# Kernel optimization log

Measured on AMD Instinct MI355X. Metric: run time of the kernel, lower is better.

The kernel has to match this reference:

```python
import jax, jax.numpy as jnp
import numpy as np

H = 100          # LSTM hidden_dim
DATA_DIM = 1500  # max_action_top(100) * max_last_action(15)
OUT = 130
B = 32           # len_batch
S = 32           # slice_index (uniform segment length)
N = 2 * B * S
RIN = 1024 + 512  # n_flatten + 512


def setup_inputs() -> dict:
    key = jax.random.key(0)
    ks = iter(jax.random.split(key, 48))
    def p(shape, s=0.05):
        return jax.random.normal(next(ks), shape, dtype=jnp.float32) * s
    inp = {
        'observations': p((N, 3, 64, 64), 1.0),
        'data': p((N, DATA_DIM), 1.0),
        'conv1_w': p((32, 3, 8, 8)), 'conv1_b': p((32,)),
        'conv2_w': p((64, 32, 4, 4)), 'conv2_b': p((64,)),
        'conv3_w': p((64, 64, 3, 3)), 'conv3_b': p((64,)),
        'lin1_w': p((1024, DATA_DIM)), 'lin1_b': p((1024,)),
        'lin2_w': p((512, 1024)), 'lin2_b': p((512,)),
        'rnns_wih0': p((4 * H, RIN)), 'rnns_whh0': p((4 * H, H)), 'rnns_bih0': p((4 * H,)), 'rnns_bhh0': p((4 * H,)),
        'rnns_wih1': p((4 * H, H)), 'rnns_whh1': p((4 * H, H)), 'rnns_bih1': p((4 * H,)), 'rnns_bhh1': p((4 * H,)),
        'rnn_wih0': p((4 * H, RIN)), 'rnn_whh0': p((4 * H, H)), 'rnn_bih0': p((4 * H,)), 'rnn_bhh0': p((4 * H,)),
        'rnn_wih1': p((4 * H, H)), 'rnn_whh1': p((4 * H, H)), 'rnn_bih1': p((4 * H,)), 'rnn_bhh1': p((4 * H,)),
        'fc1_w': p((512, 2 * H)), 'fc1_b': p((512,)),
        'fc2_w': p((OUT, 512)), 'fc2_b': p((OUT,)),
        'slice_index': S,
        'len_batch': B,
    }
    return inp


def _conv(x, w, b, stride):
    # NCHW / OIHW, VALID padding (padding=0 in torch)
    y = jax.lax.conv_general_dilated(x, w, (stride, stride), 'VALID')
    return y + b[None, :, None, None]


def _lstm_layer(x, w_ih, w_hh, b_ih, b_hh, h0, c0):
    # x: [B, S, in]; torch gate order: i, f, g, o
    bias = b_ih + b_hh
    def step(carry, x_t):
        h, c = carry
        g = x_t @ w_ih.T + h @ w_hh.T + bias
        i, f, gg, o = jnp.split(g, 4, axis=-1)
        c = jax.nn.sigmoid(f) * c + jax.nn.sigmoid(i) * jnp.tanh(gg)
        h = jax.nn.sigmoid(o) * jnp.tanh(c)
        return (h, c), h
    (hT, cT), hs = jax.lax.scan(step, (h0, c0), jnp.swapaxes(x, 0, 1))
    return jnp.swapaxes(hs, 0, 1), hT, cT


def _lstm2(x, prm, h0, c0):
    # prm: (wih0, whh0, bih0, bhh0, wih1, whh1, bih1, bhh1); h0, c0: [2, B, H]
    y0, h0f, c0f = _lstm_layer(x, prm[0], prm[1], prm[2], prm[3], h0[0], c0[0])
    y1, h1f, c1f = _lstm_layer(y0, prm[4], prm[5], prm[6], prm[7], h0[1], c0[1])
    return y1, jnp.stack([h0f, h1f]), jnp.stack([c0f, c1f])


def reference(observations, data,
              conv1_w, conv1_b, conv2_w, conv2_b, conv3_w, conv3_b,
              lin1_w, lin1_b, lin2_w, lin2_b,
              rnns_wih0, rnns_whh0, rnns_bih0, rnns_bhh0,
              rnns_wih1, rnns_whh1, rnns_bih1, rnns_bhh1,
              rnn_wih0, rnn_whh0, rnn_bih0, rnn_bhh0,
              rnn_wih1, rnn_whh1, rnn_bih1, rnn_bhh1,
              fc1_w, fc1_b, fc2_w, fc2_b,
              slice_index, len_batch):
    x = jax.nn.relu(_conv(observations, conv1_w, conv1_b, 4))
    x = jax.nn.relu(_conv(x, conv2_w, conv2_b, 2))
    x = jax.nn.relu(_conv(x, conv3_w, conv3_b, 1))
    c_out = x.reshape(x.shape[0], -1)  # [N, 1024]
    d_out = jax.nn.relu(data @ lin1_w.T + lin1_b) @ lin2_w.T + lin2_b  # [N, 512]
    feat = jnp.concatenate([c_out, d_out], axis=-1)  # [N, 1536]
    segs = feat.reshape(2 * len_batch, slice_index, feat.shape[-1])  # [2B, S, 1536]
    prm_s = (rnns_wih0, rnns_whh0, rnns_bih0, rnns_bhh0, rnns_wih1, rnns_whh1, rnns_bih1, rnns_bhh1)
    prm = (rnn_wih0, rnn_whh0, rnn_bih0, rnn_bhh0, rnn_wih1, rnn_whh1, rnn_bih1, rnn_bhh1)
    z = jnp.zeros((2, len_batch, H), dtype=feat.dtype)
    out_s, hn, cn = _lstm2(segs[:len_batch], prm_s, z, z)      # zero init, as in loop
    out, _, _ = _lstm2(segs[len_batch:], prm, hn, cn)          # carries (hn, cn) from rnn_s
    out_in = jnp.concatenate([out[:, -1, :], out_s[:, -1, :]], axis=-1)  # [B, 200]
    return jax.nn.relu(out_in @ fc1_w.T + fc1_b) @ fc2_w.T + fc2_b       # [B, OUT]
```

## Files before the change

kernel.cpp:

```cpp
#include <hip/hip_runtime.h>
#include <hip/hip_fp16.h>
#include <math.h>


typedef __attribute__((ext_vector_type(4))) float f32x4;
typedef __attribute__((ext_vector_type(8))) short s16x8;
typedef __attribute__((ext_vector_type(8))) unsigned short u16x8;
typedef __attribute__((ext_vector_type(4))) unsigned int u32x4;

__device__ __forceinline__ unsigned short f2bf(float f){
  union { float f; unsigned int u; } v; v.f = f;
  unsigned int r = (v.u + 0x7fffu + ((v.u >> 16) & 1u)) >> 16;
  return (unsigned short)r;
}
__device__ __forceinline__ unsigned short f2h(float f){
  return __half_as_ushort(__float2half(f));
}
__device__ __forceinline__ float sigmoidf_(float x){ return 1.0f/(1.0f+__expf(-x)); }
__device__ __forceinline__ float tanhf_(float x){
  float e = __expf(-2.0f*fabsf(x));
  float t = (1.0f - e)/(1.0f + e);
  return copysignf(t, x);
}

#if __has_builtin(__builtin_amdgcn_fdot2)
typedef _Float16 f16x2 __attribute__((ext_vector_type(2)));
__device__ __forceinline__ float dot2h(unsigned int a, unsigned int b, float c){
  union { unsigned int u; f16x2 h; } ua, ub;
  ua.u = a; ub.u = b;
  return __builtin_amdgcn_fdot2(ua.h, ub.h, c, false);
}
#else
__device__ __forceinline__ float dot2h(unsigned int a, unsigned int b, float c){
  __half2 ha = *(__half2*)&a, hb = *(__half2*)&b;
  float2 fa = __half22float2(ha), fb = __half22float2(hb);
  return c + fa.x*fb.x + fa.y*fb.y;
}
#endif

__global__ void prep_k(
    const float* __restrict__ data, unsigned short* __restrict__ data_bf,
    const float* __restrict__ l1w,  unsigned short* __restrict__ l1w_bf,
    const float* __restrict__ l2w,  unsigned short* __restrict__ l2w_bf,
    const float* __restrict__ c1w,  unsigned short* __restrict__ c1w_bf,
    const float* __restrict__ c2w,  unsigned short* __restrict__ c2w_bf,
    const float* __restrict__ c3w,  unsigned short* __restrict__ c3w_bf,
    const float* __restrict__ wihS, unsigned short* __restrict__ wihS_bf,
    const float* __restrict__ wihR, unsigned short* __restrict__ wihR_bf,
    const float* __restrict__ m0, const float* __restrict__ m1,
    const float* __restrict__ m2, const float* __restrict__ m3,
    const float* __restrict__ m4, const float* __restrict__ m5,
    unsigned int* __restrict__ wpk)
{
  const int job = blockIdx.y;
  const int stride = gridDim.x * blockDim.x;
  int e0 = blockIdx.x * blockDim.x + threadIdx.x;
  if (job == 0){
    for (int e = e0; e < 2048*1536; e += stride){
      int r = e / 1536, k = e - r*1536;
      data_bf[e] = (k < 1500) ? f2bf(data[(size_t)r*1500 + k]) : (unsigned short)0;
    }
  } else if (job == 1){
    for (int e = e0; e < 1024*1536; e += stride){
      int r = e / 1536, k = e - r*1536;
      l1w_bf[e] = (k < 1500) ? f2bf(l1w[(size_t)r*1500 + k]) : (unsigned short)0;
    }
  } else if (job == 2){
    for (int e = e0; e < 512*1024; e += stride) l2w_bf[e] = f2bf(l2w[e]);
  } else if (job == 3){
    for (int e = e0; e < 32*192; e += stride) c1w_bf[e] = f2bf(c1w[e]);
  } else if (job == 4){
    for (int e = e0; e < 64*512; e += stride){
      int oc = e >> 9, r = e & 511;
      int tap = r >> 5, ic = r & 31;
      c2w_bf[e] = f2bf(c2w[(size_t)oc*512 + ic*16 + tap]);
    }
  } else if (job == 5){
    for (int e = e0; e < 64*576; e += stride){
      int oc = e / 576, r = e - oc*576;
      int tap = r >> 6, ic = r & 63;
      c3w_bf[e] = f2bf(c3w[(size_t)oc*576 + ic*9 + tap]);
    }
  } else if (job == 6 || job == 7){
    const float* src = (job == 6) ? wihS : wihR;
    unsigned short* dst = (job == 6) ? wihS_bf : wihR_bf;
    for (int e = e0; e < 400*1536; e += stride){
      int g = e / 1536, k = e - g*1536;
      int ksrc = (k < 1024) ? ((k & 63)*16 + (k >> 6)) : k;
      dst[e] = f2bf(src[(size_t)g*1536 + ksrc]);
    }
  } else {
    const float* srcs[6] = {m0,m1,m2,m3,m4,m5};
    for (int e = e0; e < 6*20000; e += stride){
      int mat = e / 20000, r = e - mat*20000;
      int kk = r / 400, g = r - kk*400;
      const float* src = srcs[mat];
      unsigned int lo = f2h(src[g*100 + 2*kk]);
      unsigned int hi = f2h(src[g*100 + 2*kk + 1]);
      wpk[e] = lo | (hi << 16);
    }
  }
}

template<int BM,int BN,int WAVES_M,int WAVES_N,int AMODE,int CMODE,int RELU,int NGUARD,
         int CIN,int HI,int WI,int KH,int KW,int ST,int HO,int WO>
__global__ __launch_bounds__(256) void mgemm(
    const void* __restrict__ Av, const unsigned short* __restrict__ B,
    void* __restrict__ Cv, const float* __restrict__ bias,
    int M, int N, int K, int lda, int ldc, int cstride)
{
  constexpr int BK = 64;
  constexpr int WROWS = BM / WAVES_M;
  constexpr int WCOLS = BN / WAVES_N;
  constexpr int MF = WROWS / 16;
  constexpr int NF = WCOLS / 16;
  constexpr int HOWO = HO*WO;
  __shared__ unsigned short As[BM*BK];
  __shared__ unsigned short Bs[BN*BK];
  const int tid = threadIdx.x;
  const int bm = blockIdx.x * BM;
  const int bn = blockIdx.y * BN;
  const int lane = tid & 63, w = tid >> 6;
  const int wm = w / WAVES_N, wn = w % WAVES_N;
  const int m0 = wm * WROWS, n0 = wn * WCOLS;

  f32x4 acc[MF][NF] = {};

  const int ar = tid >> 1;
  const int as0 = 4 * (tid & 1);
  const int row_g = bm + ar;
  int a_n = 0, a_oy = 0, a_ox = 0;
  if (AMODE != 0){ a_n = row_g / HOWO; int p = row_g - a_n*HOWO; a_oy = p / WO; a_ox = p - a_oy*WO; }
// ... 87 lines not shown
  } else {
    unsigned short* tile = As;
    #pragma unroll
    for (int i = 0; i < MF; ++i)
      #pragma unroll
      for (int j = 0; j < NF; ++j){
        int col = n0 + j*16 + (lane & 15);
        float bv = bias ? bias[bn + col] : 0.f;
        #pragma unroll
        for (int q = 0; q < 4; ++q){
          int row = m0 + i*16 + (lane >> 4)*4 + q;
          float v = acc[i][j][q] + bv;
          if (RELU) v = fmaxf(v, 0.f);
          tile[row*BN + col] = f2bf(v);
        }
      }
    __syncthreads();
    unsigned short* Cu = (unsigned short*)Cv;
    constexpr int CHUNKS = (BM*BN)/(256*8);
    #pragma unroll
    for (int c = 0; c < CHUNKS; ++c){
      int flat = tid*8 + c*2048;
      int row = flat / BN, col = flat - (flat/BN)*BN;
      u16x8 v = *(const u16x8*)&tile[flat];
      int rg = bm + row;
      size_t addr;
      if constexpr (CMODE == 0) addr = (size_t)rg*ldc + bn + col;
      else { int n = rg >> 4, p = rg & 15; addr = (size_t)n*cstride + p*64 + col; }
      *(u16x8*)&Cu[addr] = v;
    }
  }
}

__global__ __launch_bounds__(256,1) void lstm_k(
    const float* __restrict__ X0s, const float* __restrict__ X0r,
    const unsigned int* __restrict__ wpk,
    const float* __restrict__ s_bih0, const float* __restrict__ s_bhh0,
    const float* __restrict__ s_bih1, const float* __restrict__ s_bhh1,
    const float* __restrict__ r_bih0, const float* __restrict__ r_bhh0,
    const float* __restrict__ r_bih1, const float* __restrict__ r_bhh1,
    const float* __restrict__ f1w, const float* __restrict__ f1b,
    const float* __restrict__ f2w, const float* __restrict__ f2b,
    float* __restrict__ out)
{
  __shared__ alignas(16) unsigned int h0p[2][56];
  __shared__ alignas(16) unsigned int h1p[2][56];
  __shared__ alignas(16) unsigned int hbufp[1792];
  __shared__ alignas(16) float Xl1[12800];
  __shared__ float xin[200];
  __shared__ float mid[512];

  const int b = blockIdx.x, tid = threadIdx.x;
  const int e = tid >> 1, sub = tid & 1;
  const bool act = (e < 100);
  const int eS = act ? e : 0;
  const int gA = sub*100 + eS;
  const int gB = gA + 200;

  if (tid < 56){ h0p[0][tid]=0u; h0p[1][tid]=0u; h1p[0][tid]=0u; h1p[1][tid]=0u; }
  for (int q = tid; q < 1792; q += 256) hbufp[q] = 0u;
  float c0r = 0.f, c1r = 0.f;
  __syncthreads();

  #pragma unroll 1
  for (int s = 0; s < 2; ++s){
    const float* Xp = (s ? X0r : X0s) + (size_t)b*32*400;
    const unsigned int* w0P  = wpk + (size_t)(s ? 3 : 0)*20000;
    const unsigned int* w1xP = wpk + (size_t)(s ? 4 : 1)*20000;
    const unsigned int* w1hP = wpk + (size_t)(s ? 5 : 2)*20000;
    const float* bi0 = s ? r_bih0 : s_bih0;
    const float* bh0 = s ? r_bhh0 : s_bhh0;
    const float* bi1 = s ? r_bih1 : s_bih1;
    const float* bh1 = s ? r_bhh1 : s_bhh1;

    {
      unsigned int wA[50], wB[50];
      #pragma unroll
      for (int p = 0; p < 50; ++p){
        wA[p] = w0P[p*400 + gA];
        wB[p] = w0P[p*400 + gB];
      }
      float bsA = bi0[gA] + bh0[gA];
      float bsB = bi0[gB] + bh0[gB];
      float xcA = Xp[gA], xcB = Xp[gB], xnA, xnB;
      #pragma unroll 1
      for (int t = 0; t < 32; ++t){
        if (t < 31){ xnA = Xp[(t+1)*400 + gA]; xnB = Xp[(t+1)*400 + gB]; }
        const u32x4* h4 = (const u32x4*)h0p[t & 1];
        float a0=0.f, a1=0.f, b0=0.f, b1=0.f;
        #pragma unroll
        for (int i = 0; i < 12; ++i){
          u32x4 hv = h4[i];
          a0 = dot2h(wA[4*i+0], hv[0], a0);
          a1 = dot2h(wA[4*i+1], hv[1], a1);
          a0 = dot2h(wA[4*i+2], hv[2], a0);
          a1 = dot2h(wA[4*i+3], hv[3], a1);
          b0 = dot2h(wB[4*i+0], hv[0], b0);
          b1 = dot2h(wB[4*i+1], hv[1], b1);
          b0 = dot2h(wB[4*i+2], hv[2], b0);
          b1 = dot2h(wB[4*i+3], hv[3], b1);
        }
        { u32x4 hv = h4[12];
          a0 = dot2h(wA[48], hv[0], a0);
          a1 = dot2h(wA[49], hv[1], a1);
          b0 = dot2h(wB[48], hv[0], b0);
          b1 = dot2h(wB[49], hv[1], b1);
        }
        float preA = (a0 + a1) + xcA + bsA;
        float preB = (b0 + b1) + xcB + bsB;
        float vA = sigmoidf_(preA);
        float vB = sub ? sigmoidf_(preB) : tanhf_(preB);
        float send = vA * vB;
        float recv = __shfl_xor(send, 1);
        if (act && sub){
          c0r = vA*c0r + recv;
          float hn = vB * tanhf_(c0r);
          unsigned short hv16 = f2h(hn);
          ((unsigned short*)h0p[(t+1) & 1])[e] = hv16;
          ((unsigned short*)hbufp)[t*112 + e] = hv16;
        }
        xcA = xnA; xcB = xnB;
        __syncthreads();
      }
    }
    {
      unsigned int wA[50], wB[50];
      #pragma unroll
      for (int p = 0; p < 50; ++p){
        wA[p] = w1xP[p*400 + gA];
        wB[p] = w1xP[p*400 + gB];
      }
      float bsA = bi1[gA] + bh1[gA];
      float bsB = bi1[gB] + bh1[gB];
      #pragma unroll 1
      for (int t = 0; t < 32; ++t){
        const u32x4* x4 = (const u32x4*)&hbufp[t*56];
        float a0=0.f, a1=0.f, b0=0.f, b1=0.f;
        #pragma unroll
        for (int i = 0; i < 12; ++i){
          u32x4 hv = x4[i];
          a0 = dot2h(wA[4*i+0], hv[0], a0);
          a1 = dot2h(wA[4*i+1], hv[1], a1);
          a0 = dot2h(wA[4*i+2], hv[2], a0);
          a1 = dot2h(wA[4*i+3], hv[3], a1);
          b0 = dot2h(wB[4*i+0], hv[0], b0);
          b1 = dot2h(wB[4*i+1], hv[1], b1);
          b0 = dot2h(wB[4*i+2], hv[2], b0);
          b1 = dot2h(wB[4*i+3], hv[3], b1);
        }
        { u32x4 hv = x4[12];
          a0 = dot2h(wA[48], hv[0], a0);
          a1 = dot2h(wA[49], hv[1], a1);
          b0 = dot2h(wB[48], hv[0], b0);
          b1 = dot2h(wB[49], hv[1], b1);
        }
        if (act){
          Xl1[t*400 + gA] = (a0 + a1) + bsA;
          Xl1[t*400 + gB] = (b0 + b1) + bsB;
        }
      }
    }
    {
      unsigned int wA[50], wB[50];
      #pragma unroll
      for (int p = 0; p < 50; ++p){
        wA[p] = w1hP[p*400 + gA];
        wB[p] = w1hP[p*400 + gB];
      }
      #pragma unroll 1
      for (int t = 0; t < 32; ++t){
        const u32x4* h4 = (const u32x4*)h1p[t & 1];
        float a0=0.f, a1=0.f, b0=0.f, b1=0.f;
        #pragma unroll
        for (int i = 0; i < 12; ++i){
          u32x4 hv = h4[i];
          a0 = dot2h(wA[4*i+0], hv[0], a0);
          a1 = dot2h(wA[4*i+1], hv[1], a1);
          a0 = dot2h(wA[4*i+2], hv[2], a0);
          a1 = dot2h(wA[4*i+3], hv[3], a1);
          b0 = dot2h(wB[4*i+0], hv[0], b0);
          b1 = dot2h(wB[4*i+1], hv[1], b1);
          b0 = dot2h(wB[4*i+2], hv[2], b0);
          b1 = dot2h(wB[4*i+3], hv[3], b1);
        }
        { u32x4 hv = h4[12];
          a0 = dot2h(wA[48], hv[0], a0);
          a1 = dot2h(wA[49], hv[1], a1);
          b0 = dot2h(wB[48], hv[0], b0);
          b1 = dot2h(wB[49], hv[1], b1);
        }
        float preA = (a0 + a1) + Xl1[t*400 + gA];
        float preB = (b0 + b1) + Xl1[t*400 + gB];
        float vA = sigmoidf_(preA);
        float vB = sub ? sigmoidf_(preB) : tanhf_(preB);
        float send = vA * vB;
        float recv = __shfl_xor(send, 1);
        if (act && sub){
          c1r = vA*c1r + recv;
          float hn = vB * tanhf_(c1r);
          ((unsigned short*)h1p[(t+1) & 1])[e] = f2h(hn);
          if (t == 31){
            if (s) xin[e] = hn;
            else   xin[100 + e] = hn;
          }
        }
        __syncthreads();
      }
    }
  }

  for (int r = tid; r < 512; r += 256){
    float acc = f1b[r];
    const float* wrow = f1w + (size_t)r*200;
    #pragma unroll 4
    for (int k = 0; k < 200; ++k) acc += xin[k]*wrow[k];
    mid[r] = fmaxf(acc, 0.f);
  }
  __syncthreads();
  if (tid < 130){
    float acc = f2b[tid];
    const float* wrow = f2w + (size_t)tid*512;
    #pragma unroll 4
    for (int k = 0; k < 512; ++k) acc += mid[k]*wrow[k];
    out[b*130 + tid] = acc;
  }
}

extern "C" void kernel_launch(void* const* d_in, const int* in_sizes, int n_in,
                              void* d_out, int out_size, void* d_ws, size_t ws_size,
                              hipStream_t stream)
{
  const float* obs  = (const float*)d_in[0];
  const float* data = (const float*)d_in[1];
  const float* c1w = (const float*)d_in[2];  const float* c1b = (const float*)d_in[3];
  const float* c2w = (const float*)d_in[4];  const float* c2b = (const float*)d_in[5];
  const float* c3w = (const float*)d_in[6];  const float* c3b = (const float*)d_in[7];
  const float* l1w = (const float*)d_in[8];  const float* l1b = (const float*)d_in[9];
  const float* l2w = (const float*)d_in[10]; const float* l2b = (const float*)d_in[11];
  const float* s_wih0=(const float*)d_in[12]; const float* s_whh0=(const float*)d_in[13];
  const float* s_bih0=(const float*)d_in[14]; const float* s_bhh0=(const float*)d_in[15];
  const float* s_wih1=(const float*)d_in[16]; const float* s_whh1=(const float*)d_in[17];
  const float* s_bih1=(const float*)d_in[18]; const float* s_bhh1=(const float*)d_in[19];
  const float* r_wih0=(const float*)d_in[20]; const float* r_whh0=(const float*)d_in[21];
  const float* r_bih0=(const float*)d_in[22]; const float* r_bhh0=(const float*)d_in[23];
  const float* r_wih1=(const float*)d_in[24]; const float* r_whh1=(const float*)d_in[25];
  const float* r_bih1=(const float*)d_in[26]; const float* r_bhh1=(const float*)d_in[27];
  const float* f1w=(const float*)d_in[28]; const float* f1b=(const float*)d_in[29];
  const float* f2w=(const float*)d_in[30]; const float* f2b=(const float*)d_in[31];
  float* out = (float*)d_out;
  (void)in_sizes; (void)n_in; (void)out_size;

  char* p = (char*)d_ws;
  auto alloc = [&](size_t bytes){ void* r = (void*)p; p += (bytes + 255) & ~(size_t)255; return r; };
  unsigned short* data_bf = (unsigned short*)alloc((size_t)2048*1536*2);
  unsigned short* c1w_bf  = (unsigned short*)alloc((size_t)32*192*2);
  unsigned short* c2w_bf  = (unsigned short*)alloc((size_t)64*512*2);
  unsigned short* c3w_bf  = (unsigned short*)alloc((size_t)64*576*2);
  unsigned short* l1w_bf  = (unsigned short*)alloc((size_t)1024*1536*2);
  unsigned short* l2w_bf  = (unsigned short*)alloc((size_t)512*1024*2);
  unsigned short* wihS_bf = (unsigned short*)alloc((size_t)400*1536*2);
  unsigned short* wihR_bf = (unsigned short*)alloc((size_t)400*1536*2);
  unsigned short* conv1o  = (unsigned short*)alloc((size_t)2048*225*32*2);
  unsigned short* conv2o  = (unsigned short*)alloc((size_t)2048*36*64*2);
  unsigned short* feat    = (unsigned short*)alloc((size_t)2048*1536*2);
  unsigned short* lin1o   = (unsigned short*)alloc((size_t)2048*1024*2);
  float* X0s  = (float*)alloc((size_t)1024*400*4);
  float* X0r  = (float*)alloc((size_t)1024*400*4);
  unsigned int* wpk = (unsigned int*)alloc((size_t)6*20000*4);
  (void)ws_size;

  prep_k<<<dim3(512,9),256,0,stream>>>(
      data, data_bf, l1w, l1w_bf, l2w, l2w_bf, c1w, c1w_bf,
      c2w, c2w_bf, c3w, c3w_bf, s_wih0, wihS_bf, r_wih0, wihR_bf,
      s_whh0, s_wih1, s_whh1, r_whh0, r_wih1, r_whh1, wpk);

  mgemm<128,32,4,1, 1,0,1,0, 3,64,64,8,8,4,15,15><<<dim3(3600,1),256,0,stream>>>(
      obs, c1w_bf, conv1o, c1b, 460800, 32, 192, 0, 32, 0);
  mgemm<128,64,2,2, 2,0,1,0, 32,15,15,4,4,2,6,6><<<dim3(576,1),256,0,stream>>>(
      conv1o, c2w_bf, conv2o, c2b, 73728, 64, 512, 0, 64, 0);
  mgemm<128,64,2,2, 0,0,1,0, 1,1,1,1,1,1,1,1><<<dim3(16,16),256,0,stream>>>(
      data_bf, l1w_bf, lin1o, l1b, 2048, 1024, 1536, 1536, 1024, 0);
  mgemm<128,64,2,2, 2,2,1,0, 64,6,6,3,3,1,4,4><<<dim3(256,1),256,0,stream>>>(
      conv2o, c3w_bf, feat, c3b, 32768, 64, 576, 0, 0, 1536);
  mgemm<128,64,2,2, 0,0,0,0, 1,1,1,1,1,1,1,1><<<dim3(16,8),256,0,stream>>>(
      lin1o, l2w_bf, feat + 1024, l2b, 2048, 512, 1024, 1024, 1536, 0);
  mgemm<128,64,2,2, 0,3,0,1, 1,1,1,1,1,1,1,1><<<dim3(8,7),256,0,stream>>>(
      feat, wihS_bf, X0s, (const float*)nullptr, 1024, 400, 1536, 1536, 400, 0);
  mgemm<128,64,2,2, 0,3,0,1, 1,1,1,1,1,1,1,1><<<dim3(8,7),256,0,stream>>>(
      feat + (size_t)1024*1536, wihR_bf, X0r, (const float*)nullptr, 1024, 400, 1536, 1536, 400, 0);

  lstm_k<<<32,256,0,stream>>>(X0s, X0r, wpk,
                              s_bih0,s_bhh0,s_bih1,s_bhh1,
                              r_bih0,r_bhh0,r_bih1,r_bhh1,
                              f1w, f1b, f2w, f2b, out);
}
```

Before: 331.5 us.

## Pipeline LSTM layers 0 and 1 across two thread groups in one block

The LSTM kernel now runs 512 threads: the first 256 compute layer 0 and the second 256 compute layer 1 one timestep behind, in a wavefront schedule. The three sequential passes (layer 0 recurrence, layer 1 input projection buffered in shared memory, layer 1 recurrence) become one loop of 33 steps. This removes the hbufp and Xl1 shared buffers and roughly halves the serial step count. In exchange, layer-1 threads hold 200 packed weight registers each, which risks spills under launch bounds of 512 threads, and layer 1 does twice the dot products per step.

```diff
diff --git a/kernel.cpp b/kernel.cpp
--- a/kernel.cpp
+++ b/kernel.cpp
@@ -251,7 +251,7 @@
   }
 }
 
-__global__ __launch_bounds__(256,1) void lstm_k(
+__global__ __launch_bounds__(512,2) void lstm_k(
     const float* __restrict__ X0s, const float* __restrict__ X0r,
     const unsigned int* __restrict__ wpk,
     const float* __restrict__ s_bih0, const float* __restrict__ s_bhh0,
@@ -264,20 +264,19 @@
 {
   __shared__ alignas(16) unsigned int h0p[2][56];
   __shared__ alignas(16) unsigned int h1p[2][56];
-  __shared__ alignas(16) unsigned int hbufp[1792];
-  __shared__ alignas(16) float Xl1[12800];
   __shared__ float xin[200];
   __shared__ float mid[512];
 
   const int b = blockIdx.x, tid = threadIdx.x;
-  const int e = tid >> 1, sub = tid & 1;
+  const bool isL0 = (tid < 256);
+  const int tl = isL0 ? tid : (tid - 256);
+  const int e = tl >> 1, sub = tl & 1;
   const bool act = (e < 100);
   const int eS = act ? e : 0;
   const int gA = sub*100 + eS;
   const int gB = gA + 200;
 
   if (tid < 56){ h0p[0][tid]=0u; h0p[1][tid]=0u; h1p[0][tid]=0u; h1p[1][tid]=0u; }
-  for (int q = tid; q < 1792; q += 256) hbufp[q] = 0u;
   float c0r = 0.f, c1r = 0.f;
   __syncthreads();
 
@@ -292,148 +291,134 @@
     const float* bi1 = s ? r_bih1 : s_bih1;
     const float* bh1 = s ? r_bhh1 : s_bhh1;
 
-    {
-      unsigned int wA[50], wB[50];
+    unsigned int wreg[200];
+    float bsA, bsB, xcA = 0.f, xcB = 0.f;
+    if (isL0){
       #pragma unroll
       for (int p = 0; p < 50; ++p){
-        wA[p] = w0P[p*400 + gA];
-        wB[p] = w0P[p*400 + gB];
-      }
-      float bsA = bi0[gA] + bh0[gA];
-      float bsB = bi0[gB] + bh0[gB];
-      float xcA = Xp[gA], xcB = Xp[gB], xnA, xnB;
-      #pragma unroll 1
-      for (int t = 0; t < 32; ++t){
-        if (t < 31){ xnA = Xp[(t+1)*400 + gA]; xnB = Xp[(t+1)*400 + gB]; }
-        const u32x4* h4 = (const u32x4*)h0p[t & 1];
-        float a0=0.f, a1=0.f, b0=0.f, b1=0.f;
-        #pragma unroll
-        for (int i = 0; i < 12; ++i){
-          u32x4 hv = h4[i];
-          a0 = dot2h(wA[4*i+0], hv[0], a0);
-          a1 = dot2h(wA[4*i+1], hv[1], a1);
-          a0 = dot2h(wA[4*i+2], hv[2], a0);
-          a1 = dot2h(wA[4*i+3], hv[3], a1);
-          b0 = dot2h(wB[4*i+0], hv[0], b0);
-          b1 = dot2h(wB[4*i+1], hv[1], b1);
-          b0 = dot2h(wB[4*i+2], hv[2], b0);
-          b1 = dot2h(wB[4*i+3], hv[3], b1);
+        wreg[p]      = w0P[p*400 + gA];
+        wreg[50+p]   = w0P[p*400 + gB];
+      }
+      bsA = bi0[gA] + bh0[gA];
+      bsB = bi0[gB] + bh0[gB];
+      xcA = Xp[gA]; xcB = Xp[gB];
+    } else {
+      #pragma unroll
+      for (int p = 0; p < 50; ++p){
+        wreg[p]      = w1hP[p*400 + gA];
+        wreg[50+p]   = w1hP[p*400 + gB];
+        wreg[100+p]  = w1xP[p*400 + gA];
+        wreg[150+p]  = w1xP[p*400 + gB];
+      }
+      bsA = bi1[gA] + bh1[gA];
+      bsB = bi1[gB] + bh1[gB];
+    }
+    __syncthreads();
+
+    #pragma unroll 1
+    for (int t = 0; t < 33; ++t){
+      if (isL0){
+        if (t < 32){
+          float xnA = 0.f, xnB = 0.f;
+          if (t < 31){ xnA = Xp[(t+1)*400 + gA]; xnB = Xp[(t+1)*400 + gB]; }
+          const u32x4* h4 = (const u32x4*)h0p[t & 1];
+          float a0=0.f, a1=0.f, b0=0.f, b1=0.f;
+          #pragma unroll
+          for (int i = 0; i < 12; ++i){
+            u32x4 hv = h4[i];
+            a0 = dot2h(wreg[4*i+0], hv[0], a0);
+            a1 = dot2h(wreg[4*i+1], hv[1], a1);
+            a0 = dot2h(wreg[4*i+2], hv[2], a0);
+            a1 = dot2h(wreg[4*i+3], hv[3], a1);
+            b0 = dot2h(wreg[50+4*i+0], hv[0], b0);
+            b1 = dot2h(wreg[50+4*i+1], hv[1], b1);
+            b0 = dot2h(wreg[50+4*i+2], hv[2], b0);
+            b1 = dot2h(wreg[50+4*i+3], hv[3], b1);
+          }
+          { u32x4 hv = h4[12];
+            a0 = dot2h(wreg[48], hv[0], a0);
+            a1 = dot2h(wreg[49], hv[1], a1);
+            b0 = dot2h(wreg[98], hv[0], b0);
+            b1 = dot2h(wreg[99], hv[1], b1);
+          }
+          float preA = (a0 + a1) + xcA + bsA;
+          float preB = (b0 + b1) + xcB + bsB;
+          float vA = sigmoidf_(preA);
+          float vB = sub ? sigmoidf_(preB) : tanhf_(preB);
+          float send = vA * vB;
+          float recv = __shfl_xor(send, 1);
+          if (act && sub){
+            c0r = vA*c0r + recv;
+            float hn = vB * tanhf_(c0r);
+            ((unsigned short*)h0p[(t+1) & 1])[e] = f2h(hn);
+          }
+          xcA = xnA; xcB = xnB;
         }
-        { u32x4 hv = h4[12];
-          a0 = dot2h(wA[48], hv[0], a0);
-          a1 = dot2h(wA[49], hv[1], a1);
-          b0 = dot2h(wB[48], hv[0], b0);
-          b1 = dot2h(wB[49], hv[1], b1);
-        }
-        float preA = (a0 + a1) + xcA + bsA;
-        float preB = (b0 + b1) + xcB + bsB;
-        float vA = sigmoidf_(preA);
-        float vB = sub ? sigmoidf_(preB) : tanhf_(preB);
-        float send = vA * vB;
-        float recv = __shfl_xor(send, 1);
-        if (act && sub){
-          c0r = vA*c0r + recv;
-          float hn = vB * tanhf_(c0r);
-          unsigned short hv16 = f2h(hn);
-          ((unsigned short*)h0p[(t+1) & 1])[e] = hv16;
-          ((unsigned short*)hbufp)[t*112 + e] = hv16;
-        }
-        xcA = xnA; xcB = xnB;
-        __syncthreads();
-      }
-    }
-    {
-      unsigned int wA[50], wB[50];
-      #pragma unroll
-      for (int p = 0; p < 50; ++p){
-        wA[p] = w1xP[p*400 + gA];
-        wB[p] = w1xP[p*400 + gB];
-      }
-      float bsA = bi1[gA] + bh1[gA];
-      float bsB = bi1[gB] + bh1[gB];
-      #pragma unroll 1
-      for (int t = 0; t < 32; ++t){
-        const u32x4* x4 = (const u32x4*)&hbufp[t*56];
-        float a0=0.f, a1=0.f, b0=0.f, b1=0.f;
-        #pragma unroll
-        for (int i = 0; i < 12; ++i){
-          u32x4 hv = x4[i];
-          a0 = dot2h(wA[4*i+0], hv[0], a0);
-          a1 = dot2h(wA[4*i+1], hv[1], a1);
-          a0 = dot2h(wA[4*i+2], hv[2], a0);
-          a1 = dot2h(wA[4*i+3], hv[3], a1);
-          b0 = dot2h(wB[4*i+0], hv[0], b0);
-          b1 = dot2h(wB[4*i+1], hv[1], b1);
-          b0 = dot2h(wB[4*i+2], hv[2], b0);
-          b1 = dot2h(wB[4*i+3], hv[3], b1);
-        }
-        { u32x4 hv = x4[12];
-          a0 = dot2h(wA[48], hv[0], a0);
-          a1 = dot2h(wA[49], hv[1], a1);
-          b0 = dot2h(wB[48], hv[0], b0);
-          b1 = dot2h(wB[49], hv[1], b1);
-        }
-        if (act){
-          Xl1[t*400 + gA] = (a0 + a1) + bsA;
-          Xl1[t*400 + gB] = (b0 + b1) + bsB;
-        }
-      }
-    }
-    {
-      unsigned int wA[50], wB[50];
-      #pragma unroll
-      for (int p = 0; p < 50; ++p){
-        wA[p] = w1hP[p*400 + gA];
-        wB[p] = w1hP[p*400 + gB];
-      }
-      #pragma unroll 1
-      for (int t = 0; t < 32; ++t){
-        const u32x4* h4 = (const u32x4*)h1p[t & 1];
-        float a0=0.f, a1=0.f, b0=0.f, b1=0.f;
-        #pragma unroll
-        for (int i = 0; i < 12; ++i){
-          u32x4 hv = h4[i];
-          a0 = dot2h(wA[4*i+0], hv[0], a0);
-          a1 = dot2h(wA[4*i+1], hv[1], a1);
-          a0 = dot2h(wA[4*i+2], hv[2], a0);
-          a1 = dot2h(wA[4*i+3], hv[3], a1);
-          b0 = dot2h(wB[4*i+0], hv[0], b0);
-          b1 = dot2h(wB[4*i+1], hv[1], b1);
-          b0 = dot2h(wB[4*i+2], hv[2], b0);
-          b1 = dot2h(wB[4*i+3], hv[3], b1);
-        }
-        { u32x4 hv = h4[12];
-          a0 = dot2h(wA[48], hv[0], a0);
-          a1 = dot2h(wA[49], hv[1], a1);
-          b0 = dot2h(wB[48], hv[0], b0);
-          b1 = dot2h(wB[49], hv[1], b1);
-        }
-        float preA = (a0 + a1) + Xl1[t*400 + gA];
-        float preB = (b0 + b1) + Xl1[t*400 + gB];
-        float vA = sigmoidf_(preA);
-        float vB = sub ? sigmoidf_(preB) : tanhf_(preB);
-        float send = vA * vB;
-        float recv = __shfl_xor(send, 1);
-        if (act && sub){
-          c1r = vA*c1r + recv;
-          float hn = vB * tanhf_(c1r);
-          ((unsigned short*)h1p[(t+1) & 1])[e] = f2h(hn);
-          if (t == 31){
-            if (s) xin[e] = hn;
-            else   xin[100 + e] = hn;
+      } else {
+        if (t >= 1){
+          const int u = t - 1;
+          const u32x4* h4 = (const u32x4*)h1p[u & 1];
+          const u32x4* x4 = (const u32x4*)h0p[t & 1];
+          float a0=0.f, a1=0.f, b0=0.f, b1=0.f;
+          #pragma unroll
+          for (int i = 0; i < 12; ++i){
+            u32x4 hv = h4[i];
+            a0 = dot2h(wreg[4*i+0], hv[0], a0);
+            a1 = dot2h(wreg[4*i+1], hv[1], a1);
+            a0 = dot2h(wreg[4*i+2], hv[2], a0);
+            a1 = dot2h(wreg[4*i+3], hv[3], a1);
+            b0 = dot2h(wreg[50+4*i+0], hv[0], b0);
+            b1 = dot2h(wreg[50+4*i+1], hv[1], b1);
+            b0 = dot2h(wreg[50+4*i+2], hv[2], b0);
+            b1 = dot2h(wreg[50+4*i+3], hv[3], b1);
+            u32x4 xv = x4[i];
+            a0 = dot2h(wreg[100+4*i+0], xv[0], a0);
+            a1 = dot2h(wreg[100+4*i+1], xv[1], a1);
+            a0 = dot2h(wreg[100+4*i+2], xv[2], a0);
+            a1 = dot2h(wreg[100+4*i+3], xv[3], a1);
+            b0 = dot2h(wreg[150+4*i+0], xv[0], b0);
+            b1 = dot2h(wreg[150+4*i+1], xv[1], b1);
+            b0 = dot2h(wreg[150+4*i+2], xv[2], b0);
+            b1 = dot2h(wreg[150+4*i+3], xv[3], b1);
+          }
+          { u32x4 hv = h4[12];
+            a0 = dot2h(wreg[48], hv[0], a0);
+            a1 = dot2h(wreg[49], hv[1], a1);
+            b0 = dot2h(wreg[98], hv[0], b0);
+            b1 = dot2h(wreg[99], hv[1], b1);
+            u32x4 xv = x4[12];
+            a0 = dot2h(wreg[148], xv[0], a0);
+            a1 = dot2h(wreg[149], xv[1], a1);
+            b0 = dot2h(wreg[198], xv[0], b0);
+            b1 = dot2h(wreg[199], xv[1], b1);
+          }
+          float preA = (a0 + a1) + bsA;
+          float preB = (b0 + b1) + bsB;
+          float vA = sigmoidf_(preA);
+          float vB = sub ? sigmoidf_(preB) : tanhf_(preB);
+          float send = vA * vB;
+          float recv = __shfl_xor(send, 1);
+          if (act && sub){
+            c1r = vA*c1r + recv;
+            float hn = vB * tanhf_(c1r);
+            ((unsigned short*)h1p[t & 1])[e] = f2h(hn);
+            if (u == 31){
+              if (s) xin[e] = hn;
+              else   xin[100 + e] = hn;
+            }
           }
         }
-        __syncthreads();
-      }
+      }
+      __syncthreads();
     }
   }
 
-  for (int r = tid; r < 512; r += 256){
-    float acc = f1b[r];
-    const float* wrow = f1w + (size_t)r*200;
+  {
+    float acc = f1b[tid];
+    const float* wrow = f1w + (size_t)tid*200;
     #pragma unroll 4
     for (int k = 0; k < 200; ++k) acc += xin[k]*wrow[k];
-    mid[r] = fmaxf(acc, 0.f);
+    mid[tid] = fmaxf(acc, 0.f);
   }
   __syncthreads();
   if (tid < 130){
@@ -508,7 +493,7 @@
   mgemm<128,64,2,2, 0,3,0,1, 1,1,1,1,1,1,1,1><<<dim3(8,7),256,0,stream>>>(
       feat + (size_t)1024*1536, wihR_bf, X0r, (const float*)nullptr, 1024, 400, 1536, 1536, 400, 0);
 
-  lstm_k<<<32,256,0,stream>>>(X0s, X0r, wpk,
+  lstm_k<<<32,512,0,stream>>>(X0s, X0r, wpk,
                               s_bih0,s_bhh0,s_bih1,s_bhh1,
                               r_bih0,r_bhh0,r_bih1,r_bhh1,
                               f1w, f1b, f2w, f2b, out);
```

After: 697.3 us. 110% more time.

## Pack four LSTM sequences per 1024-thread block and store layer-1 inputs as fp16

Applied to the files above, without the earlier changes.

The LSTM kernel now runs four batch sequences in one 1024-thread block (8 blocks instead of 32). Each 256-thread slice keeps its own shared-memory hidden-state buffers. The precomputed layer-1 input projections are stored as fp16 instead of fp32 so that four slices fit in LDS. The intent appears to be fewer blocks that share weight fetches through cache. The costs are block-wide barriers across 1024 threads, a 128-VGPR limit per thread that may spill the 100 register-resident weights, and lower precision for the layer-1 inputs.

```diff
diff --git a/kernel.cpp b/kernel.cpp
--- a/kernel.cpp
+++ b/kernel.cpp
@@ -15,6 +15,9 @@
 }
 __device__ __forceinline__ unsigned short f2h(float f){
   return __half_as_ushort(__float2half(f));
+}
+__device__ __forceinline__ float h2f(unsigned short u){
+  return __half2float(__ushort_as_half(u));
 }
 __device__ __forceinline__ float sigmoidf_(float x){ return 1.0f/(1.0f+__expf(-x)); }
 __device__ __forceinline__ float tanhf_(float x){
@@ -251,7 +254,8 @@
   }
 }
 
-__global__ __launch_bounds__(256,1) void lstm_k(
+#define NSEG 4
+__global__ __launch_bounds__(1024,1) void lstm_k(
     const float* __restrict__ X0s, const float* __restrict__ X0r,
     const unsigned int* __restrict__ wpk,
     const float* __restrict__ s_bih0, const float* __restrict__ s_bhh0,
@@ -262,22 +266,25 @@
     const float* __restrict__ f2w, const float* __restrict__ f2b,
     float* __restrict__ out)
 {
-  __shared__ alignas(16) unsigned int h0p[2][56];
-  __shared__ alignas(16) unsigned int h1p[2][56];
-  __shared__ alignas(16) unsigned int hbufp[1792];
-  __shared__ alignas(16) float Xl1[12800];
-  __shared__ float xin[200];
-  __shared__ float mid[512];
-
-  const int b = blockIdx.x, tid = threadIdx.x;
-  const int e = tid >> 1, sub = tid & 1;
+  __shared__ alignas(16) unsigned int h0p[NSEG][2][56];
+  __shared__ alignas(16) unsigned int h1p[NSEG][2][56];
+  __shared__ alignas(16) unsigned int hbufp[NSEG][1792];
+  __shared__ alignas(16) unsigned short Xl1h[NSEG][12800];
+  __shared__ float xin[NSEG][200];
+  __shared__ float mid[NSEG][512];
+
+  const int tid = threadIdx.x;
+  const int sl = tid >> 8;
+  const int tl = tid & 255;
+  const int b = blockIdx.x*NSEG + sl;
+  const int e = tl >> 1, sub = tl & 1;
   const bool act = (e < 100);
   const int eS = act ? e : 0;
   const int gA = sub*100 + eS;
   const int gB = gA + 200;
 
-  if (tid < 56){ h0p[0][tid]=0u; h0p[1][tid]=0u; h1p[0][tid]=0u; h1p[1][tid]=0u; }
-  for (int q = tid; q < 1792; q += 256) hbufp[q] = 0u;
+  if (tl < 56){ h0p[sl][0][tl]=0u; h0p[sl][1][tl]=0u; h1p[sl][0][tl]=0u; h1p[sl][1][tl]=0u; }
+  for (int q = tl; q < 1792; q += 256) hbufp[sl][q] = 0u;
   float c0r = 0.f, c1r = 0.f;
   __syncthreads();
 
@@ -305,7 +312,7 @@
       #pragma unroll 1
       for (int t = 0; t < 32; ++t){
         if (t < 31){ xnA = Xp[(t+1)*400 + gA]; xnB = Xp[(t+1)*400 + gB]; }
-        const u32x4* h4 = (const u32x4*)h0p[t & 1];
+        const u32x4* h4 = (const u32x4*)h0p[sl][t & 1];
         float a0=0.f, a1=0.f, b0=0.f, b1=0.f;
         #pragma unroll
         for (int i = 0; i < 12; ++i){
@@ -335,8 +342,8 @@
           c0r = vA*c0r + recv;
           float hn = vB * tanhf_(c0r);
           unsigned short hv16 = f2h(hn);
-          ((unsigned short*)h0p[(t+1) & 1])[e] = hv16;
-          ((unsigned short*)hbufp)[t*112 + e] = hv16;
+          ((unsigned short*)h0p[sl][(t+1) & 1])[e] = hv16;
+          ((unsigned short*)hbufp[sl])[t*112 + e] = hv16;
         }
         xcA = xnA; xcB = xnB;
         __syncthreads();
@@ -353,7 +360,7 @@
       float bsB = bi1[gB] + bh1[gB];
       #pragma unroll 1
       for (int t = 0; t < 32; ++t){
-        const u32x4* x4 = (const u32x4*)&hbufp[t*56];
+        const u32x4* x4 = (const u32x4*)&hbufp[sl][t*56];
         float a0=0.f, a1=0.f, b0=0.f, b1=0.f;
         #pragma unroll
         for (int i = 0; i < 12; ++i){
@@ -374,8 +381,8 @@
           b1 = dot2h(wB[49], hv[1], b1);
         }
         if (act){
-          Xl1[t*400 + gA] = (a0 + a1) + bsA;
-          Xl1[t*400 + gB] = (b0 + b1) + bsB;
+          Xl1h[sl][t*400 + gA] = f2h((a0 + a1) + bsA);
+          Xl1h[sl][t*400 + gB] = f2h((b0 + b1) + bsB);
         }
       }
     }
@@ -388,7 +395,7 @@
       }
       #pragma unroll 1
       for (int t = 0; t < 32; ++t){
-        const u32x4* h4 = (const u32x4*)h1p[t & 1];
+        const u32x4* h4 = (const u32x4*)h1p[sl][t & 1];
         float a0=0.f, a1=0.f, b0=0.f, b1=0.f;
         #pragma unroll
         for (int i = 0; i < 12; ++i){
@@ -408,8 +415,8 @@
           b0 = dot2h(wB[48], hv[0], b0);
           b1 = dot2h(wB[49], hv[1], b1);
         }
-        float preA = (a0 + a1) + Xl1[t*400 + gA];
-        float preB = (b0 + b1) + Xl1[t*400 + gB];
+        float preA = (a0 + a1) + h2f(Xl1h[sl][t*400 + gA]);
+        float preB = (b0 + b1) + h2f(Xl1h[sl][t*400 + gB]);
         float vA = sigmoidf_(preA);
         float vB = sub ? sigmoidf_(preB) : tanhf_(preB);
         float send = vA * vB;
@@ -417,10 +424,10 @@
         if (act && sub){
           c1r = vA*c1r + recv;
           float hn = vB * tanhf_(c1r);
-          ((unsigned short*)h1p[(t+1) & 1])[e] = f2h(hn);
+          ((unsigned short*)h1p[sl][(t+1) & 1])[e] = f2h(hn);
           if (t == 31){
-            if (s) xin[e] = hn;
-            else   xin[100 + e] = hn;
+            if (s) xin[sl][e] = hn;
+            else   xin[sl][100 + e] = hn;
           }
         }
         __syncthreads();
@@ -428,20 +435,20 @@
     }
   }
 
-  for (int r = tid; r < 512; r += 256){
+  for (int r = tl; r < 512; r += 256){
     float acc = f1b[r];
     const float* wrow = f1w + (size_t)r*200;
     #pragma unroll 4
-    for (int k = 0; k < 200; ++k) acc += xin[k]*wrow[k];
-    mid[r] = fmaxf(acc, 0.f);
+    for (int k = 0; k < 200; ++k) acc += xin[sl][k]*wrow[k];
+    mid[sl][r] = fmaxf(acc, 0.f);
   }
   __syncthreads();
-  if (tid < 130){
-    float acc = f2b[tid];
-    const float* wrow = f2w + (size_t)tid*512;
+  if (tl < 130){
+    float acc = f2b[tl];
+    const float* wrow = f2w + (size_t)tl*512;
     #pragma unroll 4
-    for (int k = 0; k < 512; ++k) acc += mid[k]*wrow[k];
-    out[b*130 + tid] = acc;
+    for (int k = 0; k < 512; ++k) acc += mid[sl][k]*wrow[k];
+    out[b*130 + tl] = acc;
   }
 }
 
@@ -508,7 +515,7 @@
   mgemm<128,64,2,2, 0,3,0,1, 1,1,1,1,1,1,1,1><<<dim3(8,7),256,0,stream>>>(
       feat + (size_t)1024*1536, wihR_bf, X0r, (const float*)nullptr, 1024, 400, 1536, 1536, 400, 0);
 
-  lstm_k<<<32,256,0,stream>>>(X0s, X0r, wpk,
+  lstm_k<<<8,1024,0,stream>>>(X0s, X0r, wpk,
                               s_bih0,s_bhh0,s_bih1,s_bhh1,
                               r_bih0,r_bhh0,r_bih1,r_bhh1,
                               f1w, f1b, f2w, f2b, out);
```

New measurement: 1.087 ms. +227.9%, slower.

## Split LSTM into wavefront kernels and move layer-1 input projection to GEMM

Applied to the files above, without the earlier changes.

The single LSTM kernel used to run four recurrences back to back: both layers of rnn_s, then both layers of rnn. It is now split into three recurrence kernels with GEMM launches between them. The layer-1 input projections become bf16 matrix-core GEMMs over the stored layer-0 hidden states, and layer-1 of rnn_s runs in the same launch as layer-0 of rnn. This cuts the serial chain from four 32-step recurrences to three and takes the scalar input projection off the critical path. In exchange it adds more kernel launches, extra global round trips for hidden states, carried state and projections, and bf16 rounding of layer-0 outputs.

```diff
diff --git a/kernel.cpp b/kernel.cpp
--- a/kernel.cpp
+++ b/kernel.cpp
@@ -49,8 +49,16 @@
     const float* __restrict__ wihR, unsigned short* __restrict__ wihR_bf,
     const float* __restrict__ m0, const float* __restrict__ m1,
     const float* __restrict__ m2, const float* __restrict__ m3,
-    const float* __restrict__ m4, const float* __restrict__ m5,
-    unsigned int* __restrict__ wpk)
+    unsigned int* __restrict__ wpk,
+    const float* __restrict__ wih1S, const float* __restrict__ wih1R,
+    unsigned short* __restrict__ w1xS_bf, unsigned short* __restrict__ w1xR_bf,
+    const float* __restrict__ s_bih0, const float* __restrict__ s_bhh0,
+    const float* __restrict__ s_bih1, const float* __restrict__ s_bhh1,
+    const float* __restrict__ r_bih0, const float* __restrict__ r_bhh0,
+    const float* __restrict__ r_bih1, const float* __restrict__ r_bhh1,
+    float* __restrict__ bias0S, float* __restrict__ bias0R,
+    float* __restrict__ bias1S, float* __restrict__ bias1R,
+    unsigned short* __restrict__ h0outS, unsigned short* __restrict__ h0outR)
 {
   const int job = blockIdx.y;
   const int stride = gridDim.x * blockDim.x;
@@ -89,15 +97,35 @@
       int ksrc = (k < 1024) ? ((k & 63)*16 + (k >> 6)) : k;
       dst[e] = f2bf(src[(size_t)g*1536 + ksrc]);
     }
-  } else {
-    const float* srcs[6] = {m0,m1,m2,m3,m4,m5};
-    for (int e = e0; e < 6*20000; e += stride){
+  } else if (job == 8){
+    const float* srcs[4] = {m0,m1,m2,m3};
+    for (int e = e0; e < 4*20000; e += stride){
       int mat = e / 20000, r = e - mat*20000;
       int kk = r / 400, g = r - kk*400;
       const float* src = srcs[mat];
       unsigned int lo = f2h(src[g*100 + 2*kk]);
       unsigned int hi = f2h(src[g*100 + 2*kk + 1]);
       wpk[e] = lo | (hi << 16);
+    }
+  } else if (job == 9){
+    for (int e = e0; e < 2*400*128; e += stride){
+      int half = e / 51200, r = e - half*51200;
+      int g = r >> 7, k = r & 127;
+      const float* src = half ? wih1R : wih1S;
+      unsigned short* dst = half ? w1xR_bf : w1xS_bf;
+      dst[r] = (k < 100) ? f2bf(src[g*100 + k]) : (unsigned short)0;
+    }
+  } else {
+    for (int e = e0; e < 1600 + 131072; e += stride){
+      if (e < 400)        bias0S[e]       = s_bih0[e]       + s_bhh0[e];
+      else if (e < 800)   bias0R[e-400]   = r_bih0[e-400]   + r_bhh0[e-400];
+      else if (e < 1200)  bias1S[e-800]   = s_bih1[e-800]   + s_bhh1[e-800];
+      else if (e < 1600)  bias1R[e-1200]  = r_bih1[e-1200]  + r_bhh1[e-1200];
+      else {
+        int idx = e - 1600;
+        if (idx < 65536) ((unsigned int*)h0outS)[idx] = 0u;
+        else             ((unsigned int*)h0outR)[idx - 65536] = 0u;
+      }
     }
   }
 }
@@ -251,183 +279,142 @@
   }
 }
 
-__global__ __launch_bounds__(256,1) void lstm_k(
-    const float* __restrict__ X0s, const float* __restrict__ X0r,
-    const unsigned int* __restrict__ wpk,
-    const float* __restrict__ s_bih0, const float* __restrict__ s_bhh0,
-    const float* __restrict__ s_bih1, const float* __restrict__ s_bhh1,
-    const float* __restrict__ r_bih0, const float* __restrict__ r_bhh0,
-    const float* __restrict__ r_bih1, const float* __restrict__ r_bhh1,
-    const float* __restrict__ f1w, const float* __restrict__ f1b,
-    const float* __restrict__ f2w, const float* __restrict__ f2b,
-    float* __restrict__ out)
-{
-  __shared__ alignas(16) unsigned int h0p[2][56];
-  __shared__ alignas(16) unsigned int h1p[2][56];
-  __shared__ alignas(16) unsigned int hbufp[1792];
-  __shared__ alignas(16) float Xl1[12800];
-  __shared__ float xin[200];
-  __shared__ float mid[512];
-
-  const int b = blockIdx.x, tid = threadIdx.x;
+__device__ __forceinline__ void rec_body(
+    int seg, int tid,
+    const float* __restrict__ X,
+    const unsigned int* __restrict__ wP,
+    const float* __restrict__ bsum,
+    const float* __restrict__ hinit,
+    const float* __restrict__ cinit,
+    unsigned short* __restrict__ houtm,
+    float* __restrict__ hfin,
+    float* __restrict__ cfin,
+    unsigned int (*hp)[56],
+    float* __restrict__ xout)
+{
   const int e = tid >> 1, sub = tid & 1;
   const bool act = (e < 100);
   const int eS = act ? e : 0;
   const int gA = sub*100 + eS;
   const int gB = gA + 200;
 
-  if (tid < 56){ h0p[0][tid]=0u; h0p[1][tid]=0u; h1p[0][tid]=0u; h1p[1][tid]=0u; }
-  for (int q = tid; q < 1792; q += 256) hbufp[q] = 0u;
-  float c0r = 0.f, c1r = 0.f;
+  if (tid < 56){
+    unsigned int v = 0u;
+    if (hinit && tid < 50){
+      unsigned int lo = f2h(hinit[seg*100 + 2*tid]);
+      unsigned int hi = f2h(hinit[seg*100 + 2*tid + 1]);
+      v = lo | (hi << 16);
+    }
+    hp[0][tid] = v;
+    hp[1][tid] = 0u;
+  }
+  float cr = 0.f;
+  if (cinit && act && sub) cr = cinit[seg*100 + e];
   __syncthreads();
 
+  unsigned int wA[50], wB[50];
+  #pragma unroll
+  for (int p = 0; p < 50; ++p){
+    wA[p] = wP[p*400 + gA];
+    wB[p] = wP[p*400 + gB];
+  }
+  float bsA = bsum ? bsum[gA] : 0.f;
+  float bsB = bsum ? bsum[gB] : 0.f;
+  const float* Xs = X + (size_t)seg*32*400;
+  float xcA = Xs[gA], xcB = Xs[gB], xnA = 0.f, xnB = 0.f;
+  float hnK = 0.f;
+
   #pragma unroll 1
-  for (int s = 0; s < 2; ++s){
-    const float* Xp = (s ? X0r : X0s) + (size_t)b*32*400;
-    const unsigned int* w0P  = wpk + (size_t)(s ? 3 : 0)*20000;
-    const unsigned int* w1xP = wpk + (size_t)(s ? 4 : 1)*20000;
-    const unsigned int* w1hP = wpk + (size_t)(s ? 5 : 2)*20000;
-    const float* bi0 = s ? r_bih0 : s_bih0;
-    const float* bh0 = s ? r_bhh0 : s_bhh0;
-    const float* bi1 = s ? r_bih1 : s_bih1;
-    const float* bh1 = s ? r_bhh1 : s_bhh1;
-
-    {
-      unsigned int wA[50], wB[50];
-      #pragma unroll
-      for (int p = 0; p < 50; ++p){
-        wA[p] = w0P[p*400 + gA];
-        wB[p] = w0P[p*400 + gB];
-      }
-      float bsA = bi0[gA] + bh0[gA];
-      float bsB = bi0[gB] + bh0[gB];
-      float xcA = Xp[gA], xcB = Xp[gB], xnA, xnB;
-      #pragma unroll 1
-      for (int t = 0; t < 32; ++t){
-        if (t < 31){ xnA = Xp[(t+1)*400 + gA]; xnB = Xp[(t+1)*400 + gB]; }
-        const u32x4* h4 = (const u32x4*)h0p[t & 1];
-        float a0=0.f, a1=0.f, b0=0.f, b1=0.f;
-        #pragma unroll
-        for (int i = 0; i < 12; ++i){
-          u32x4 hv = h4[i];
-          a0 = dot2h(wA[4*i+0], hv[0], a0);
-          a1 = dot2h(wA[4*i+1], hv[1], a1);
-          a0 = dot2h(wA[4*i+2], hv[2], a0);
-          a1 = dot2h(wA[4*i+3], hv[3], a1);
-          b0 = dot2h(wB[4*i+0], hv[0], b0);
-          b1 = dot2h(wB[4*i+1], hv[1], b1);
-          b0 = dot2h(wB[4*i+2], hv[2], b0);
-          b1 = dot2h(wB[4*i+3], hv[3], b1);
-        }
-        { u32x4 hv = h4[12];
-          a0 = dot2h(wA[48], hv[0], a0);
-          a1 = dot2h(wA[49], hv[1], a1);
-          b0 = dot2h(wB[48], hv[0], b0);
-          b1 = dot2h(wB[49], hv[1], b1);
-        }
-        float preA = (a0 + a1) + xcA + bsA;
-        float preB = (b0 + b1) + xcB + bsB;
-        float vA = sigmoidf_(preA);
-        float vB = sub ? sigmoidf_(preB) : tanhf_(preB);
-        float send = vA * vB;
-        float recv = __shfl_xor(send, 1);
-        if (act && sub){
-          c0r = vA*c0r + recv;
-          float hn = vB * tanhf_(c0r);
-          unsigned short hv16 = f2h(hn);
-          ((unsigned short*)h0p[(t+1) & 1])[e] = hv16;
-          ((unsigned short*)hbufp)[t*112 + e] = hv16;
-        }
-        xcA = xnA; xcB = xnB;
-        __syncthreads();
-      }
-    }
-    {
-      unsigned int wA[50], wB[50];
-      #pragma unroll
-      for (int p = 0; p < 50; ++p){
-        wA[p] = w1xP[p*400 + gA];
-        wB[p] = w1xP[p*400 + gB];
-      }
-      float bsA = bi1[gA] + bh1[gA];
-      float bsB = bi1[gB] + bh1[gB];
-      #pragma unroll 1
-      for (int t = 0; t < 32; ++t){
-        const u32x4* x4 = (const u32x4*)&hbufp[t*56];
-        float a0=0.f, a1=0.f, b0=0.f, b1=0.f;
-        #pragma unroll
-        for (int i = 0; i < 12; ++i){
-          u32x4 hv = x4[i];
-          a0 = dot2h(wA[4*i+0], hv[0], a0);
-          a1 = dot2h(wA[4*i+1], hv[1], a1);
-          a0 = dot2h(wA[4*i+2], hv[2], a0);
-          a1 = dot2h(wA[4*i+3], hv[3], a1);
-          b0 = dot2h(wB[4*i+0], hv[0], b0);
-          b1 = dot2h(wB[4*i+1], hv[1], b1);
-          b0 = dot2h(wB[4*i+2], hv[2], b0);
-          b1 = dot2h(wB[4*i+3], hv[3], b1);
-        }
-        { u32x4 hv = x4[12];
-          a0 = dot2h(wA[48], hv[0], a0);
-          a1 = dot2h(wA[49], hv[1], a1);
-          b0 = dot2h(wB[48], hv[0], b0);
-          b1 = dot2h(wB[49], hv[1], b1);
-        }
-        if (act){
-          Xl1[t*400 + gA] = (a0 + a1) + bsA;
-          Xl1[t*400 + gB] = (b0 + b1) + bsB;
-        }
-      }
-    }
-    {
-      unsigned int wA[50], wB[50];
-      #pragma unroll
-      for (int p = 0; p < 50; ++p){
-        wA[p] = w1hP[p*400 + gA];
-        wB[p] = w1hP[p*400 + gB];
-      }
-      #pragma unroll 1
-      for (int t = 0; t < 32; ++t){
-        const u32x4* h4 = (const u32x4*)h1p[t & 1];
-        float a0=0.f, a1=0.f, b0=0.f, b1=0.f;
-        #pragma unroll
-        for (int i = 0; i < 12; ++i){
-          u32x4 hv = h4[i];
-          a0 = dot2h(wA[4*i+0], hv[0], a0);
-          a1 = dot2h(wA[4*i+1], hv[1], a1);
-          a0 = dot2h(wA[4*i+2], hv[2], a0);
-          a1 = dot2h(wA[4*i+3], hv[3], a1);
-          b0 = dot2h(wB[4*i+0], hv[0], b0);
-          b1 = dot2h(wB[4*i+1], hv[1], b1);
-          b0 = dot2h(wB[4*i+2], hv[2], b0);
-          b1 = dot2h(wB[4*i+3], hv[3], b1);
-        }
-        { u32x4 hv = h4[12];
-          a0 = dot2h(wA[48], hv[0], a0);
-          a1 = dot2h(wA[49], hv[1], a1);
-          b0 = dot2h(wB[48], hv[0], b0);
-          b1 = dot2h(wB[49], hv[1], b1);
-        }
-        float preA = (a0 + a1) + Xl1[t*400 + gA];
-        float preB = (b0 + b1) + Xl1[t*400 + gB];
-        float vA = sigmoidf_(preA);
-        float vB = sub ? sigmoidf_(preB) : tanhf_(preB);
-        float send = vA * vB;
-        float recv = __shfl_xor(send, 1);
-        if (act && sub){
-          c1r = vA*c1r + recv;
-          float hn = vB * tanhf_(c1r);
-          ((unsigned short*)h1p[(t+1) & 1])[e] = f2h(hn);
-          if (t == 31){
-            if (s) xin[e] = hn;
-            else   xin[100 + e] = hn;
-          }
-        }
-        __syncthreads();
-      }
-    }
-  }
-
+  for (int t = 0; t < 32; ++t){
+    if (t < 31){ xnA = Xs[(t+1)*400 + gA]; xnB = Xs[(t+1)*400 + gB]; }
+    const u32x4* h4 = (const u32x4*)hp[t & 1];
+    float a0=0.f, a1=0.f, b0=0.f, b1=0.f;
+    #pragma unroll
+    for (int i = 0; i < 12; ++i){
+      u32x4 hv = h4[i];
+      a0 = dot2h(wA[4*i+0], hv[0], a0);
+      a1 = dot2h(wA[4*i+1], hv[1], a1);
+      a0 = dot2h(wA[4*i+2], hv[2], a0);
+      a1 = dot2h(wA[4*i+3], hv[3], a1);
+      b0 = dot2h(wB[4*i+0], hv[0], b0);
+      b1 = dot2h(wB[4*i+1], hv[1], b1);
+      b0 = dot2h(wB[4*i+2], hv[2], b0);
+      b1 = dot2h(wB[4*i+3], hv[3], b1);
+    }
+    { u32x4 hv = h4[12];
+      a0 = dot2h(wA[48], hv[0], a0);
+      a1 = dot2h(wA[49], hv[1], a1);
+      b0 = dot2h(wB[48], hv[0], b0);
+      b1 = dot2h(wB[49], hv[1], b1);
+    }
+    float preA = (a0 + a1) + xcA + bsA;
+    float preB = (b0 + b1) + xcB + bsB;
+    float vA = sigmoidf_(preA);
+    float vB = sub ? sigmoidf_(preB) : tanhf_(preB);
+    float send = vA * vB;
+    float recv = __shfl_xor(send, 1);
+    if (act && sub){
+      cr = vA*cr + recv;
+      float hn = vB * tanhf_(cr);
+      hnK = hn;
+      ((unsigned short*)hp[(t+1) & 1])[e] = f2h(hn);
+      if (houtm) houtm[((size_t)seg*32 + t)*128 + e] = f2bf(hn);
+    }
+    xcA = xnA; xcB = xnB;
+    __syncthreads();
+  }
+
+  if (act && sub){
+    if (hfin) hfin[seg*100 + e] = hnK;
+    if (cfin) cfin[seg*100 + e] = cr;
+    if (xout) xout[e] = hnK;
+  }
+}
+
+__global__ __launch_bounds__(256,1) void recA_k(
+    const float* __restrict__ X0s, const unsigned int* __restrict__ wpk,
+    const float* __restrict__ bias0S,
+    unsigned short* __restrict__ h0outS,
+    float* __restrict__ h0finS, float* __restrict__ c0finS)
+{
+  __shared__ unsigned int hp[2][56];
+  rec_body(blockIdx.x, threadIdx.x, X0s, wpk, bias0S, nullptr, nullptr,
+           h0outS, h0finS, c0finS, hp, nullptr);
+}
+
+__global__ __launch_bounds__(256,1) void recB_k(
+    const float* __restrict__ X1s, const float* __restrict__ X0r,
+    const unsigned int* __restrict__ wpk, const float* __restrict__ bias0R,
+    const float* __restrict__ h0finS, const float* __restrict__ c0finS,
+    unsigned short* __restrict__ h0outR,
+    float* __restrict__ h1finS, float* __restrict__ c1finS)
+{
+  __shared__ unsigned int hp[2][56];
+  int bx = blockIdx.x;
+  if (bx < 32){
+    rec_body(bx, threadIdx.x, X1s, wpk + 20000, nullptr, nullptr, nullptr,
+             nullptr, h1finS, c1finS, hp, nullptr);
+  } else {
+    rec_body(bx - 32, threadIdx.x, X0r, wpk + 40000, bias0R, h0finS, c0finS,
+             h0outR, nullptr, nullptr, hp, nullptr);
+  }
+}
+
+__global__ __launch_bounds__(256,1) void recC_k(
+    const float* __restrict__ X1r, const unsigned int* __restrict__ wpk,
+    const float* __restrict__ h1finS, const float* __restrict__ c1finS,
+    const float* __restrict__ f1w, const float* __restrict__ f1b,
+    const float* __restrict__ f2w, const float* __restrict__ f2b,
+    float* __restrict__ out)
+{
+  __shared__ unsigned int hp[2][56];
+  __shared__ float xin[208];
+  __shared__ float mid[512];
+  const int tid = threadIdx.x, b = blockIdx.x;
+  rec_body(b, tid, X1r, wpk + 60000, nullptr, h1finS, c1finS,
+           nullptr, nullptr, nullptr, hp, xin);
+  if (tid < 100) xin[100 + tid] = h1finS[b*100 + tid];
+  __syncthreads();
   for (int r = tid; r < 512; r += 256){
     float acc = f1b[r];
     const float* wrow = f1w + (size_t)r*200;
@@ -485,13 +472,30 @@
   unsigned short* lin1o   = (unsigned short*)alloc((size_t)2048*1024*2);
   float* X0s  = (float*)alloc((size_t)1024*400*4);
   float* X0r  = (float*)alloc((size_t)1024*400*4);
-  unsigned int* wpk = (unsigned int*)alloc((size_t)6*20000*4);
+  unsigned int* wpk = (unsigned int*)alloc((size_t)4*20000*4);
+  unsigned short* w1xS_bf = (unsigned short*)alloc((size_t)400*128*2);
+  unsigned short* w1xR_bf = (unsigned short*)alloc((size_t)400*128*2);
+  unsigned short* h0outS  = (unsigned short*)alloc((size_t)1024*128*2);
+  unsigned short* h0outR  = (unsigned short*)alloc((size_t)1024*128*2);
+  float* X1s = (float*)alloc((size_t)1024*400*4);
+  float* X1r = (float*)alloc((size_t)1024*400*4);
+  float* bias0S = (float*)alloc(400*4);
+  float* bias0R = (float*)alloc(400*4);
+  float* bias1S = (float*)alloc(400*4);
+  float* bias1R = (float*)alloc(400*4);
+  float* h0finS = (float*)alloc(3200*4);
+  float* c0finS = (float*)alloc(3200*4);
+  float* h1finS = (float*)alloc(3200*4);
+  float* c1finS = (float*)alloc(3200*4);
   (void)ws_size;
 
-  prep_k<<<dim3(512,9),256,0,stream>>>(
+  prep_k<<<dim3(512,11),256,0,stream>>>(
       data, data_bf, l1w, l1w_bf, l2w, l2w_bf, c1w, c1w_bf,
       c2w, c2w_bf, c3w, c3w_bf, s_wih0, wihS_bf, r_wih0, wihR_bf,
-      s_whh0, s_wih1, s_whh1, r_whh0, r_wih1, r_whh1, wpk);
+      s_whh0, s_whh1, r_whh0, r_whh1, wpk,
+      s_wih1, r_wih1, w1xS_bf, w1xR_bf,
+      s_bih0, s_bhh0, s_bih1, s_bhh1, r_bih0, r_bhh0, r_bih1, r_bhh1,
+      bias0S, bias0R, bias1S, bias1R, h0outS, h0outR);
 
   mgemm<128,32,4,1, 1,0,1,0, 3,64,64,8,8,4,15,15><<<dim3(3600,1),256,0,stream>>>(
       obs, c1w_bf, conv1o, c1b, 460800, 32, 192, 0, 32, 0);
@@ -508,8 +512,13 @@
   mgemm<128,64,2,2, 0,3,0,1, 1,1,1,1,1,1,1,1><<<dim3(8,7),256,0,stream>>>(
       feat + (size_t)1024*1536, wihR_bf, X0r, (const float*)nullptr, 1024, 400, 1536, 1536, 400, 0);
 
-  lstm_k<<<32,256,0,stream>>>(X0s, X0r, wpk,
-                              s_bih0,s_bhh0,s_bih1,s_bhh1,
-                              r_bih0,r_bhh0,r_bih1,r_bhh1,
+  recA_k<<<32,256,0,stream>>>(X0s, wpk, bias0S, h0outS, h0finS, c0finS);
+  mgemm<128,64,2,2, 0,3,0,1, 1,1,1,1,1,1,1,1><<<dim3(8,7),256,0,stream>>>(
+      h0outS, w1xS_bf, X1s, bias1S, 1024, 400, 128, 128, 400, 0);
+  recB_k<<<64,256,0,stream>>>(X1s, X0r, wpk, bias0R, h0finS, c0finS,
+                              h0outR, h1finS, c1finS);
+  mgemm<128,64,2,2, 0,3,0,1, 1,1,1,1,1,1,1,1><<<dim3(8,7),256,0,stream>>>(
+      h0outR, w1xR_bf, X1r, bias1R, 1024, 400, 128, 128, 400, 0);
+  recC_k<<<32,256,0,stream>>>(X1r, wpk, h1finS, c1finS,
                               f1w, f1b, f2w, f2b, out);
 }
```

Measured after the change: 301.6 us. 1.1x faster.
